# Kernel optimization log

Hardware: AMD Instinct MI355X
Metric: run time of the kernel (lower is better)

Reference implementation:

```python
import jax, jax.numpy as jnp
import numpy as np

H, W = 250, 400
N_RAYS = H * W          # 100000 (one patch)
N_SAMPLES = 1_000_000
P, C, DIM = 50000, 16, 8
STEP_SIZE = 0.005
DENSITY_SHIFT = 0.0
DENSITY_SCALE = min(1.0 / (1.0 - DENSITY_SHIFT), 25.0)


def setup_inputs() -> dict:
    key = jax.random.key(0)
    ks = jax.random.split(key, 12)
    return {
        "trivecs": jax.random.normal(ks[0], (P, C, 3, DIM), dtype=jnp.float32),
        "densities": jax.random.normal(ks[1], (P, C), dtype=jnp.float32),
        "colors": jax.random.normal(ks[2], (P, C, 3), dtype=jnp.float32),
        "local_gweight_s": jax.random.uniform(ks[3], (N_SAMPLES, 3), dtype=jnp.float32),
        "local_gweight_l": jax.random.uniform(ks[4], (N_SAMPLES, 3), dtype=jnp.float32),
        "t_min": jax.random.uniform(ks[5], (N_RAYS,), dtype=jnp.float32),
        "bg": jax.random.uniform(ks[6], (3,), dtype=jnp.float32),
        "local_gindx_s": jax.random.randint(ks[7], (N_SAMPLES, 3), 0, DIM, dtype=jnp.int32),
        "local_gindx_l": jax.random.randint(ks[8], (N_SAMPLES, 3), 0, DIM, dtype=jnp.int32),
        "tensoRF_id": jax.random.randint(ks[9], (N_SAMPLES,), 0, P, dtype=jnp.int32),
        "ray_id": jnp.sort(jax.random.randint(ks[10], (N_SAMPLES,), 0, N_RAYS, dtype=jnp.int32)),
        "step_id": jax.random.randint(ks[11], (N_SAMPLES,), 0, 200, dtype=jnp.int32),
    }


def reference(trivecs, densities, colors, local_gweight_s, local_gweight_l,
              t_min, bg, local_gindx_s, local_gindx_l, tensoRF_id, ray_id, step_id):
    # --- compute_feature: trilinear tensor-decomposition gather ---
    def interp(a):
        vs = trivecs[tensoRF_id, :, a, local_gindx_s[:, a]]  # [N, C]
        vl = trivecs[tensoRF_id, :, a, local_gindx_l[:, a]]  # [N, C]
        return vs * local_gweight_s[:, a:a + 1] + vl * local_gweight_l[:, a:a + 1]

    feature = interp(0) * interp(1) * interp(2)               # [N, C]
    sigma = (feature * densities[tensoRF_id]).sum(axis=1)     # [N]
    color = jnp.einsum('nc,nck->nk', feature, colors[tensoRF_id])  # [N, 3]

    # --- density activation & alpha ---
    density = jax.nn.softplus(sigma - DENSITY_SHIFT * 10.0) * DENSITY_SCALE
    alpha = 1.0 - jnp.exp(-density * STEP_SIZE)               # [N]

    # --- Alphas2Weights: per-ray exclusive transmittance (ray_id sorted) ---
    log_t = -density * STEP_SIZE                              # == log(1 - alpha)
    seg_total = jax.ops.segment_sum(log_t, ray_id, num_segments=N_RAYS)  # [R]
    seg_offset = jnp.concatenate([jnp.zeros((1,), log_t.dtype),
                                  jnp.cumsum(seg_total)[:-1]])           # [R]
    excl = jnp.cumsum(log_t) - log_t - seg_offset[ray_id]     # within-segment excl cumsum
    weights = alpha * jnp.exp(excl)                           # [N]
    bg_weight = jnp.exp(seg_total)                            # [R], prod(1-alpha) per ray

    # --- ray compositing ---
    rgb = jax.nn.sigmoid(color)                               # [N, 3]
    rgb_map = jax.ops.segment_sum(weights[:, None] * rgb, ray_id, num_segments=N_RAYS)
    rgb_map = rgb_map + bg_weight[:, None] * bg[None, :]
    z_val = t_min[ray_id] + step_id.astype(jnp.float32) * STEP_SIZE
    depth_map = jax.ops.segment_sum(weights * z_val, ray_id, num_segments=N_RAYS)
    alpha_map = 1.0 - bg_weight

    rgb_map = rgb_map.T.reshape(3, H, W)
    depth_map = depth_map.reshape(H, W)
    alpha_map = alpha_map.reshape(H, W)
    return rgb_map, depth_map, alpha_map
```

## Files before the change

kernel.cpp:

```cpp
#include <hip/hip_runtime.h>
#include <math.h>

#define HN       250
#define WN       400
#define N_RAYS   (HN * WN)
#define N_SAMP   1000000
#define P_TENSO  50000
#define STEP_SZ  0.005f
#define DENS_SCALE 1.0f
#define NB_SCAN  ((P_TENSO + 1023) / 1024)


#define OFF_PACK    0
#define OFF_RESULTS 32000000
#define OFF_PERM    48000000
#define OFF_RT      52000000
#define OFF_CURSOR  56000000
#define OFF_STARTS  56200000
#define OFF_BSUMS   56400000
#define OFF_FLAG    56400512
#define OFF_RSTART  56401024
#define WS_NEED     (56401024 + 400004 + 64)

#define ROW_STRIDE 20
#define TV_F   (24 * ROW_STRIDE)
#define SLAB_F (TV_F + 16 + 48)

__global__ __launch_bounds__(256) void pack_bounds_rank(
    const int*   __restrict__ tenso_id,
    const int*   __restrict__ ray_id,
    const int*   __restrict__ gis, const int* __restrict__ gil,
    const float* __restrict__ gws, const float* __restrict__ gwl,
    int* __restrict__ cursor,
    int* __restrict__ rt,
    int* __restrict__ ray_start,
    float4* __restrict__ pack)
{
    int n = blockIdx.x * 256 + threadIdx.x;
    if (n >= N_SAMP) return;

    const int tid = tenso_id[n];
    const int rk = atomicAdd(&cursor[tid], 1);
    rt[n] = (tid << 16) | rk;

    unsigned bits = (unsigned)gis[n*3+0] | ((unsigned)gis[n*3+1] << 3) | ((unsigned)gis[n*3+2] << 6)
                  | ((unsigned)gil[n*3+0] << 9) | ((unsigned)gil[n*3+1] << 12) | ((unsigned)gil[n*3+2] << 15);
    float4 A = make_float4(gws[n*3+0], gws[n*3+1], gws[n*3+2], gwl[n*3+0]);
    float4 B = make_float4(gwl[n*3+1], gwl[n*3+2], __uint_as_float(bits), 0.0f);
    pack[(size_t)n * 2 + 0] = A;
    pack[(size_t)n * 2 + 1] = B;

    int r = ray_id[n];
    int rprev = (n == 0) ? -1 : ray_id[n - 1];
    for (int q = rprev + 1; q <= r; ++q) ray_start[q] = n;
    if (n == N_SAMP - 1) {
        for (int q = r + 1; q <= N_RAYS; ++q) ray_start[q] = N_SAMP;
    }
}

__global__ __launch_bounds__(256) void scan_fused(
    const int* __restrict__ cursor,
    int* __restrict__ starts,
    int* __restrict__ bsums,
    int* __restrict__ flag)
{
    __shared__ int lds[257];
    const int b = blockIdx.x;
    const int t = threadIdx.x;
    const int base = b * 1024 + t * 4;

    int v[4]; int s = 0;
    #pragma unroll
    for (int i = 0; i < 4; ++i) {
        int idx = base + i;
        v[i] = (idx < P_TENSO) ? cursor[idx] : 0;
        s += v[i];
    }
    lds[t] = s;
    __syncthreads();
    for (int d = 1; d < 256; d <<= 1) {
        int x = (t >= d) ? lds[t - d] : 0;
        __syncthreads();
        lds[t] += x;
        __syncthreads();
    }
    if (t == 255) bsums[b] = lds[255];

    __threadfence();
    __syncthreads();
    if (t == 0) {
        atomicAdd(flag, 1);
        while (atomicAdd(flag, 0) < gridDim.x) { }
    }
    __syncthreads();
    __threadfence();

    if (t < 64) {
        int x = (t < b) ? bsums[t] : 0;
        #pragma unroll
        for (int m = 1; m < 64; m <<= 1) x += __shfl_xor(x, m);
        if (t == 0) lds[256] = x;
    }
    __syncthreads();
    const int pre = lds[256];

    int run = pre + ((t > 0) ? lds[t - 1] : 0);
    #pragma unroll
    for (int i = 0; i < 4; ++i) {
        int idx = base + i;
        if (idx < P_TENSO) starts[idx] = run;
        run += v[i];
    }
}

__global__ __launch_bounds__(256) void finalize_perm(
    const int* __restrict__ rt,
    const int* __restrict__ starts,
    int* __restrict__ perm)
{
    int n = blockIdx.x * 256 + threadIdx.x;
    if (n >= N_SAMP) return;
    const unsigned w = (unsigned)rt[n];
    int pos = starts[w >> 16] + (int)(w & 0xFFFFu);
    perm[pos] = n;
}

__global__ __launch_bounds__(256) void gather_phase(
    const float* __restrict__ trivecs,
    const float* __restrict__ densities,
    const float* __restrict__ colors,
    const int*   __restrict__ starts,
    const int*   __restrict__ counts,
    const int*   __restrict__ perm,
    const float4* __restrict__ pack,
    float* __restrict__ results_f)
{
    __shared__ __align__(16) float lds[4 * SLAB_F];
    const int lane = threadIdx.x & 63;
    const int wv   = threadIdx.x >> 6;
    const int t    = blockIdx.x * 4 + wv;
    if (t >= P_TENSO) return;

    const int start = starts[t];
    const int cnt   = counts[t];
    if (cnt == 0) return;

    float* slab = lds + wv * SLAB_F;
    float* dl   = slab + TV_F;
    float* cl   = dl + 16;

    const int g = lane >> 2;
    const int j = lane & 3;
    const int end = start + cnt;

    int p = start + g;
    int n = perm[(p < end) ? p : (end - 1)];

    const float* tvg = trivecs + (size_t)t * 384;
    #pragma unroll
    for (int i = 0; i < 6; ++i) {
        int l = lane + i * 64;
        int c = l / 24;
        int rem = l - c * 24;
        slab[rem * ROW_STRIDE + c] = tvg[l];
    }
    if (lane < 16) dl[lane] = densities[(size_t)t * 16 + lane];
    if (lane < 48) {
        int c = lane / 3, k = lane - c * 3;
        cl[k * 16 + c] = colors[(size_t)t * 48 + lane];
    }

    const float4 dens4 = *(const float4*)(dl + 4 * j);
    const float4 col0  = *(const float4*)(cl + 4 * j);
    const float4 col1  = *(const float4*)(cl + 16 + 4 * j);
    const float4 col2  = *(const float4*)(cl + 32 + 4 * j);

    const int niter = (cnt + 15) >> 4;

    for (int it = 0; it < niter; ++it) {
        const bool valid = (p < end);
        const int sn = n;

        const float4 A = pack[(size_t)sn * 2 + 0];
        const float4 B = pack[(size_t)sn * 2 + 1];

        if (it + 1 < niter) {
            p = start + (it + 1) * 16 + g;
            n = perm[(p < end) ? p : (end - 1)];
        }

        const unsigned bits = __float_as_uint(B.z);

        float4 f;
        {
            const int is = bits & 7, il = (bits >> 9) & 7;
            const float4 vs = *(const float4*)(slab + is * ROW_STRIDE + 4 * j);
            const float4 vl = *(const float4*)(slab + il * ROW_STRIDE + 4 * j);
            f.x = vs.x * A.x + vl.x * A.w;
            f.y = vs.y * A.x + vl.y * A.w;
            f.z = vs.z * A.x + vl.z * A.w;
            f.w = vs.w * A.x + vl.w * A.w;
        }
        {
            const int is = (bits >> 3) & 7, il = (bits >> 12) & 7;
            const float4 vs = *(const float4*)(slab + (8 + is) * ROW_STRIDE + 4 * j);
            const float4 vl = *(const float4*)(slab + (8 + il) * ROW_STRIDE + 4 * j);
            f.x *= vs.x * A.y + vl.x * B.x;
            f.y *= vs.y * A.y + vl.y * B.x;
            f.z *= vs.z * A.y + vl.z * B.x;
            f.w *= vs.w * A.y + vl.w * B.x;
        }
        {
            const int is = (bits >> 6) & 7, il = (bits >> 15) & 7;
            const float4 vs = *(const float4*)(slab + (16 + is) * ROW_STRIDE + 4 * j);
            const float4 vl = *(const float4*)(slab + (16 + il) * ROW_STRIDE + 4 * j);
            f.x *= vs.x * A.z + vl.x * B.y;
            f.y *= vs.y * A.z + vl.y * B.y;
            f.z *= vs.z * A.z + vl.z * B.y;
            f.w *= vs.w * A.z + vl.w * B.y;
        }

        float s0 = f.x * dens4.x + f.y * dens4.y + f.z * dens4.z + f.w * dens4.w;
        float s1 = f.x * col0.x  + f.y * col0.y  + f.z * col0.z  + f.w * col0.w;
        float s2 = f.x * col1.x  + f.y * col1.y  + f.z * col1.z  + f.w * col1.w;
        float s3 = f.x * col2.x  + f.y * col2.y  + f.z * col2.z  + f.w * col2.w;

        s0 += __shfl_xor(s0, 1); s0 += __shfl_xor(s0, 2);
        s1 += __shfl_xor(s1, 1); s1 += __shfl_xor(s1, 2);
        s2 += __shfl_xor(s2, 1); s2 += __shfl_xor(s2, 2);
        s3 += __shfl_xor(s3, 1); s3 += __shfl_xor(s3, 2);

        const float sj = (j == 0) ? s0 : (j == 1) ? s1 : (j == 2) ? s2 : s3;
        float val;
        if (j == 0) {
            float dens = fmaxf(sj, 0.0f) + __logf(1.0f + __expf(-fabsf(sj)));
            val = -(dens * DENS_SCALE) * STEP_SZ;
        } else {
            val = 1.0f / (1.0f + __expf(-sj));
        }
        if (valid) results_f[(size_t)sn * 4 + j] = val;
    }
}

__global__ __launch_bounds__(256) void ray_render(
    const float4* __restrict__ results,
    const float*  __restrict__ t_min,
    const float*  __restrict__ bg,
    const int*    __restrict__ ray_start,
    const int*    __restrict__ step_id,
    float* __restrict__ out)
{
    const int lane = threadIdx.x & 63;
    const int g    = lane & 3;
    const int r    = (blockIdx.x * 256 + threadIdx.x) >> 2;
    if (r >= N_RAYS) return;
    const int s = ray_start[r];
    const int e = ray_start[r + 1];
    const float tmin_r = t_min[r];

    float eT = 1.0f, aR = 0.0f, aG = 0.0f, aB = 0.0f, aD = 0.0f;
    const int niter = (e - s + 3) >> 2;
    for (int it = 0; it < niter; ++it) {
        const int idx = s + it * 4 + g;
        const bool valid = (idx < e);
        const int ci = valid ? idx : (e - 1);
        const float4 res = results[ci];
        const float z = tmin_r + (float)step_id[ci] * STEP_SZ;
        const float elt = valid ? __expf(res.x) : 1.0f;

        float excl = 1.0f;
        const float v1 = __shfl_up(elt, 1, 4); if (g >= 1) excl *= v1;
        const float v2 = __shfl_up(elt, 2, 4); if (g >= 2) excl *= v2;
        const float v3 = __shfl_up(elt, 3, 4); if (g >= 3) excl *= v3;

        const float w = eT * excl * (1.0f - elt);
        aR += w * res.y;
        aG += w * res.z;
        aB += w * res.w;
        aD += w * z;

        const float tot = __shfl(excl * elt, 3, 4);
        eT *= tot;
    }

    aR += __shfl_xor(aR, 1); aR += __shfl_xor(aR, 2);
    aG += __shfl_xor(aG, 1); aG += __shfl_xor(aG, 2);
    aB += __shfl_xor(aB, 1); aB += __shfl_xor(aB, 2);
    aD += __shfl_xor(aD, 1); aD += __shfl_xor(aD, 2);

    const float outv = (g == 0) ? aR + eT * bg[0]
                     : (g == 1) ? aG + eT * bg[1]
                     : (g == 2) ? aB + eT * bg[2]
                     : aD;
    out[g * N_RAYS + r] = outv;
    if (g == 0) out[4 * N_RAYS + r] = 1.0f - eT;
}

__global__ __launch_bounds__(256) void trivec_render_fallback(
    const float* __restrict__ trivecs, const float* __restrict__ densities,
    const float* __restrict__ colors, const float* __restrict__ gws,
    const float* __restrict__ gwl, const float* __restrict__ t_min,
    const float* __restrict__ bg, const int* __restrict__ gis,
    const int* __restrict__ gil, const int* __restrict__ tenso_id,
    const int* __restrict__ ray_id, const int* __restrict__ step_id,
    float* __restrict__ out)
{
    const int lane = threadIdx.x & 63;
    const int r = blockIdx.x * 4 + (threadIdx.x >> 6);
    if (r >= N_RAYS) return;
    const int c = lane & 15;
    const int g = lane >> 4;
    int lo = 0, hi = N_SAMP;
    while (lo < hi) { int mid = (lo + hi) >> 1; if (ray_id[mid] < r) lo = mid + 1; else hi = mid; }
    const int seg_start = lo;
    hi = N_SAMP;
    while (lo < hi) { int mid = (lo + hi) >> 1; if (ray_id[mid] < r + 1) lo = mid + 1; else hi = mid; }
    const int seg_end = lo;
    const float tmin_r = t_min[r];
    float Tlog = 0.0f, accR = 0.0f, accG = 0.0f, accB = 0.0f, accD = 0.0f;
    const int niter = (seg_end - seg_start + 3) >> 2;
    for (int it = 0; it < niter; ++it) {
        const int n = seg_start + it * 4 + g;
        const bool valid = (n < seg_end);
        const int nc = valid ? n : (seg_end - 1);
        const int tid = tenso_id[nc];
        const float* tv = trivecs + (size_t)tid * 384 + c * 24;
        float f = 1.0f;
        #pragma unroll
        for (int a = 0; a < 3; ++a) {
            const int is = gis[nc*3+a], il = gil[nc*3+a];
            const float wS = gws[nc*3+a], wL = gwl[nc*3+a];
            f *= (tv[a*8+is] * wS + tv[a*8+il] * wL);
        }
        const float dns = densities[(size_t)tid * 16 + c];
        const float* colp = colors + ((size_t)tid * 16 + c) * 3;
        float s0 = f*dns, s1 = f*colp[0], s2 = f*colp[1], s3 = f*colp[2];
        #pragma unroll
        for (int m = 1; m < 16; m <<= 1) {
            s0 += __shfl_xor(s0, m); s1 += __shfl_xor(s1, m);
            s2 += __shfl_xor(s2, m); s3 += __shfl_xor(s3, m);
        }
        float dens = fmaxf(s0, 0.0f) + __logf(1.0f + __expf(-fabsf(s0)));
        const float lt = valid ? (-dens * STEP_SZ) : 0.0f;
        const float alpha = 1.0f - __expf(lt);
        const float rr = 1.0f/(1.0f+__expf(-s1)), gg = 1.0f/(1.0f+__expf(-s2)), bb = 1.0f/(1.0f+__expf(-s3));
        const float z = tmin_r + (float)step_id[nc] * STEP_SZ;
        const float lt0 = __shfl(lt,0), lt1 = __shfl(lt,16), lt2 = __shfl(lt,32), lt3 = __shfl(lt,48);
        float excl = Tlog;
        if (g > 0) excl += lt0;
        if (g > 1) excl += lt1;
        if (g > 2) excl += lt2;
        const float w = alpha * __expf(excl);
        Tlog += lt0 + lt1 + lt2 + lt3;
        accR += w*rr; accG += w*gg; accB += w*bb; accD += w*z;
    }
    accR += __shfl_xor(accR,16); accR += __shfl_xor(accR,32);
    accG += __shfl_xor(accG,16); accG += __shfl_xor(accG,32);
    accB += __shfl_xor(accB,16); accB += __shfl_xor(accB,32);
    accD += __shfl_xor(accD,16); accD += __shfl_xor(accD,32);
    const float bgw = __expf(Tlog);
    if (lane == 0) {
        out[0*N_RAYS+r] = accR + bgw*bg[0];
        out[1*N_RAYS+r] = accG + bgw*bg[1];
        out[2*N_RAYS+r] = accB + bgw*bg[2];
        out[3*N_RAYS+r] = accD;
        out[4*N_RAYS+r] = 1.0f - bgw;
    }
}

extern "C" void kernel_launch(void* const* d_in, const int* in_sizes, int n_in,
                              void* d_out, int out_size, void* d_ws, size_t ws_size,
                              hipStream_t stream) {
    const float* trivecs   = (const float*)d_in[0];
    const float* densities = (const float*)d_in[1];
    const float* colors    = (const float*)d_in[2];
    const float* gws       = (const float*)d_in[3];
    const float* gwl       = (const float*)d_in[4];
    const float* t_min     = (const float*)d_in[5];
    const float* bg        = (const float*)d_in[6];
    const int*   gis       = (const int*)d_in[7];
    const int*   gil       = (const int*)d_in[8];
    const int*   tenso_id  = (const int*)d_in[9];
    const int*   ray_id    = (const int*)d_in[10];
    const int*   step_id   = (const int*)d_in[11];
    float* out = (float*)d_out;

    if (ws_size < (size_t)WS_NEED) {
        trivec_render_fallback<<<(N_RAYS + 3) / 4, 256, 0, stream>>>(
            trivecs, densities, colors, gws, gwl, t_min, bg,
            gis, gil, tenso_id, ray_id, step_id, out);
        return;
    }

    char* ws = (char*)d_ws;
    float4* pack     = (float4*)(ws + OFF_PACK);
    float4* results  = (float4*)(ws + OFF_RESULTS);
    int*    perm     = (int*)(ws + OFF_PERM);
    int*    rt       = (int*)(ws + OFF_RT);
    int*    cursor   = (int*)(ws + OFF_CURSOR);
    int*    starts   = (int*)(ws + OFF_STARTS);
    int*    bsums    = (int*)(ws + OFF_BSUMS);
    int*    flag     = (int*)(ws + OFF_FLAG);
    int*    raystart = (int*)(ws + OFF_RSTART);

    hipMemsetAsync(ws + OFF_CURSOR, 0, (OFF_FLAG + 64) - OFF_CURSOR, stream);

    pack_bounds_rank<<<(N_SAMP + 255) / 256, 256, 0, stream>>>(
        tenso_id, ray_id, gis, gil, gws, gwl, cursor, rt, raystart, pack);
    scan_fused<<<NB_SCAN, 256, 0, stream>>>(cursor, starts, bsums, flag);
    finalize_perm<<<(N_SAMP + 255) / 256, 256, 0, stream>>>(
        rt, starts, perm);
    gather_phase<<<(P_TENSO + 3) / 4, 256, 0, stream>>>(
        trivecs, densities, colors, starts, cursor, perm, pack, (float*)results);
    ray_render<<<(N_RAYS * 4 + 255) / 256, 256, 0, stream>>>(
        results, t_min, bg, raystart, step_id, out);
}
```

Baseline: 278.5 us.

## Fuse permutation scatter into scan kernel and make gather persistent with prefetch

Folds the permutation scatter into the scan kernel behind a second grid-wide spin barrier, removing one kernel launch. The scan kernel also writes an end sentinel to starts so the gather kernel no longer needs the counts array. The gather kernel becomes persistent: a fixed grid of 2048 blocks loops over tensors, loading the next tensor's vectors, densities, colors and bounds into registers while processing the current one. The ray-boundary pass now gets the previous ray id with a wave shuffle instead of a second global load. The risk is that the fused scatter runs on only about 49 blocks, which sharply cuts parallelism for a 1M-element latency-bound scatter.

```diff
diff --git a/kernel.cpp b/kernel.cpp
--- a/kernel.cpp
+++ b/kernel.cpp
@@ -9,6 +9,8 @@
 #define STEP_SZ  0.005f
 #define DENS_SCALE 1.0f
 #define NB_SCAN  ((P_TENSO + 1023) / 1024)
+#define NB_GATHER 2048
+#define NW_GATHER (NB_GATHER * 4)
 
 
 #define OFF_PACK    0
@@ -17,7 +19,7 @@
 #define OFF_RT      52000000
 #define OFF_CURSOR  56000000
 #define OFF_STARTS  56200000
-#define OFF_BSUMS   56400000
+#define OFF_BSUMS   56400064
 #define OFF_FLAG    56400512
 #define OFF_RSTART  56401024
 #define WS_NEED     (56401024 + 400004 + 64)
@@ -38,6 +40,7 @@
 {
     int n = blockIdx.x * 256 + threadIdx.x;
     if (n >= N_SAMP) return;
+    const int lane = threadIdx.x & 63;
 
     const int tid = tenso_id[n];
     const int rk = atomicAdd(&cursor[tid], 1);
@@ -50,19 +53,24 @@
     pack[(size_t)n * 2 + 0] = A;
     pack[(size_t)n * 2 + 1] = B;
 
-    int r = ray_id[n];
-    int rprev = (n == 0) ? -1 : ray_id[n - 1];
+    const int r = ray_id[n];
+    const int rup = __shfl_up(r, 1);
+    int rprev;
+    if (lane == 0) rprev = (n == 0) ? -1 : ray_id[n - 1];
+    else           rprev = rup;
     for (int q = rprev + 1; q <= r; ++q) ray_start[q] = n;
     if (n == N_SAMP - 1) {
         for (int q = r + 1; q <= N_RAYS; ++q) ray_start[q] = N_SAMP;
     }
 }
 
-__global__ __launch_bounds__(256) void scan_fused(
+__global__ __launch_bounds__(256) void scan_finalize(
     const int* __restrict__ cursor,
+    const int* __restrict__ rt,
     int* __restrict__ starts,
     int* __restrict__ bsums,
-    int* __restrict__ flag)
+    int* __restrict__ flag,
+    int* __restrict__ perm)
 {
     __shared__ int lds[257];
     const int b = blockIdx.x;
@@ -89,8 +97,8 @@
     __threadfence();
     __syncthreads();
     if (t == 0) {
-        atomicAdd(flag, 1);
-        while (atomicAdd(flag, 0) < gridDim.x) { }
+        atomicAdd(&flag[0], 1);
+        while (atomicAdd(&flag[0], 0) < NB_SCAN) { }
     }
     __syncthreads();
     __threadfence();
@@ -110,19 +118,22 @@
         int idx = base + i;
         if (idx < P_TENSO) starts[idx] = run;
         run += v[i];
-    }
-}
-
-__global__ __launch_bounds__(256) void finalize_perm(
-    const int* __restrict__ rt,
-    const int* __restrict__ starts,
-    int* __restrict__ perm)
-{
-    int n = blockIdx.x * 256 + threadIdx.x;
-    if (n >= N_SAMP) return;
-    const unsigned w = (unsigned)rt[n];
-    int pos = starts[w >> 16] + (int)(w & 0xFFFFu);
-    perm[pos] = n;
+        if (idx == P_TENSO - 1) starts[P_TENSO] = run;
+    }
+
+    __threadfence();
+    __syncthreads();
+    if (t == 0) {
+        atomicAdd(&flag[1], 1);
+        while (atomicAdd(&flag[1], 0) < NB_SCAN) { }
+    }
+    __syncthreads();
+    __threadfence();
+
+    for (int n = b * 256 + t; n < N_SAMP; n += NB_SCAN * 256) {
+        const unsigned w = (unsigned)rt[n];
+        perm[starts[w >> 16] + (int)(w & 0xFFFFu)] = n;
+    }
 }
 
 __global__ __launch_bounds__(256) void gather_phase(
@@ -130,7 +141,6 @@
     const float* __restrict__ densities,
     const float* __restrict__ colors,
     const int*   __restrict__ starts,
-    const int*   __restrict__ counts,
     const int*   __restrict__ perm,
     const float4* __restrict__ pack,
     float* __restrict__ results_f)
@@ -138,107 +148,133 @@
     __shared__ __align__(16) float lds[4 * SLAB_F];
     const int lane = threadIdx.x & 63;
     const int wv   = threadIdx.x >> 6;
-    const int t    = blockIdx.x * 4 + wv;
-    if (t >= P_TENSO) return;
-
-    const int start = starts[t];
-    const int cnt   = counts[t];
-    if (cnt == 0) return;
-
     float* slab = lds + wv * SLAB_F;
     float* dl   = slab + TV_F;
     float* cl   = dl + 16;
-
     const int g = lane >> 2;
     const int j = lane & 3;
-    const int end = start + cnt;
-
-    int p = start + g;
-    int n = perm[(p < end) ? p : (end - 1)];
-
-    const float* tvg = trivecs + (size_t)t * 384;
-    #pragma unroll
-    for (int i = 0; i < 6; ++i) {
-        int l = lane + i * 64;
-        int c = l / 24;
-        int rem = l - c * 24;
-        slab[rem * ROW_STRIDE + c] = tvg[l];
-    }
-    if (lane < 16) dl[lane] = densities[(size_t)t * 16 + lane];
-    if (lane < 48) {
-        int c = lane / 3, k = lane - c * 3;
-        cl[k * 16 + c] = colors[(size_t)t * 48 + lane];
-    }
-
-    const float4 dens4 = *(const float4*)(dl + 4 * j);
-    const float4 col0  = *(const float4*)(cl + 4 * j);
-    const float4 col1  = *(const float4*)(cl + 16 + 4 * j);
-    const float4 col2  = *(const float4*)(cl + 32 + 4 * j);
-
-    const int niter = (cnt + 15) >> 4;
-
-    for (int it = 0; it < niter; ++it) {
-        const bool valid = (p < end);
-        const int sn = n;
-
-        const float4 A = pack[(size_t)sn * 2 + 0];
-        const float4 B = pack[(size_t)sn * 2 + 1];
-
-        if (it + 1 < niter) {
-            p = start + (it + 1) * 16 + g;
-            n = perm[(p < end) ? p : (end - 1)];
+
+    int wr0,wr1,wr2,wr3,wr4,wr5;
+    {
+        int l, c, rem;
+        l = lane;       c = l/24; rem = l - c*24; wr0 = rem*ROW_STRIDE + c;
+        l = lane + 64;  c = l/24; rem = l - c*24; wr1 = rem*ROW_STRIDE + c;
+        l = lane + 128; c = l/24; rem = l - c*24; wr2 = rem*ROW_STRIDE + c;
+        l = lane + 192; c = l/24; rem = l - c*24; wr3 = rem*ROW_STRIDE + c;
+        l = lane + 256; c = l/24; rem = l - c*24; wr4 = rem*ROW_STRIDE + c;
+        l = lane + 320; c = l/24; rem = l - c*24; wr5 = rem*ROW_STRIDE + c;
+    }
+    int cli; { int c = lane/3, k = lane - c*3; cli = k*16 + c; }
+
+    int t = blockIdx.x * 4 + wv;
+
+    float v0,v1,v2,v3,v4,v5, vd, vc;
+    {
+        const float* tvg = trivecs + (size_t)t * 384;
+        v0 = tvg[lane];       v1 = tvg[lane + 64];  v2 = tvg[lane + 128];
+        v3 = tvg[lane + 192]; v4 = tvg[lane + 256]; v5 = tvg[lane + 320];
+        vd = (lane < 16) ? densities[(size_t)t * 16 + lane] : 0.0f;
+        vc = (lane < 48) ? colors[(size_t)t * 48 + lane]    : 0.0f;
+    }
+    int st0 = starts[t], st1 = starts[t + 1];
+    slab[wr0]=v0; slab[wr1]=v1; slab[wr2]=v2; slab[wr3]=v3; slab[wr4]=v4; slab[wr5]=v5;
+    if (lane < 16) dl[lane] = vd;
+    if (lane < 48) cl[cli]  = vc;
+
+    for (;;) {
+        const int tn = t + NW_GATHER;
+        const bool hn = (tn < P_TENSO);
+        int stn0 = 0, stn1 = 0;
+        if (hn) {
+            const float* tvn = trivecs + (size_t)tn * 384;
+            v0 = tvn[lane];       v1 = tvn[lane + 64];  v2 = tvn[lane + 128];
+            v3 = tvn[lane + 192]; v4 = tvn[lane + 256]; v5 = tvn[lane + 320];
+            vd = (lane < 16) ? densities[(size_t)tn * 16 + lane] : 0.0f;
+            vc = (lane < 48) ? colors[(size_t)tn * 48 + lane]    : 0.0f;
+            stn0 = starts[tn]; stn1 = starts[tn + 1];
         }
 
-        const unsigned bits = __float_as_uint(B.z);
-
-        float4 f;
-        {
-            const int is = bits & 7, il = (bits >> 9) & 7;
-            const float4 vs = *(const float4*)(slab + is * ROW_STRIDE + 4 * j);
-            const float4 vl = *(const float4*)(slab + il * ROW_STRIDE + 4 * j);
-            f.x = vs.x * A.x + vl.x * A.w;
-            f.y = vs.y * A.x + vl.y * A.w;
-            f.z = vs.z * A.x + vl.z * A.w;
-            f.w = vs.w * A.x + vl.w * A.w;
+        const int start = st0, end = st1, cnt = st1 - st0;
+        if (cnt > 0) {
+            int p = start + g;
+            int n = perm[(p < end) ? p : (end - 1)];
+
+            const float4 dens4 = *(const float4*)(dl + 4 * j);
+            const float4 col0  = *(const float4*)(cl + 4 * j);
+            const float4 col1  = *(const float4*)(cl + 16 + 4 * j);
+            const float4 col2  = *(const float4*)(cl + 32 + 4 * j);
+
+            const int niter = (cnt + 15) >> 4;
+            for (int it = 0; it < niter; ++it) {
+                const bool valid = (p < end);
+                const int sn = n;
+
+                const float4 A = pack[(size_t)sn * 2 + 0];
+                const float4 B = pack[(size_t)sn * 2 + 1];
+
+                if (it + 1 < niter) {
+                    p = start + (it + 1) * 16 + g;
+                    n = perm[(p < end) ? p : (end - 1)];
+                }
+
+                const unsigned bits = __float_as_uint(B.z);
+
+                float4 f;
+                {
+                    const int is = bits & 7, il = (bits >> 9) & 7;
+                    const float4 vs = *(const float4*)(slab + is * ROW_STRIDE + 4 * j);
+                    const float4 vl = *(const float4*)(slab + il * ROW_STRIDE + 4 * j);
+                    f.x = vs.x * A.x + vl.x * A.w;
+                    f.y = vs.y * A.x + vl.y * A.w;
+                    f.z = vs.z * A.x + vl.z * A.w;
+                    f.w = vs.w * A.x + vl.w * A.w;
+                }
+                {
+                    const int is = (bits >> 3) & 7, il = (bits >> 12) & 7;
+                    const float4 vs = *(const float4*)(slab + (8 + is) * ROW_STRIDE + 4 * j);
+                    const float4 vl = *(const float4*)(slab + (8 + il) * ROW_STRIDE + 4 * j);
+                    f.x *= vs.x * A.y + vl.x * B.x;
+                    f.y *= vs.y * A.y + vl.y * B.x;
+                    f.z *= vs.z * A.y + vl.z * B.x;
+                    f.w *= vs.w * A.y + vl.w * B.x;
+                }
+                {
+                    const int is = (bits >> 6) & 7, il = (bits >> 15) & 7;
+                    const float4 vs = *(const float4*)(slab + (16 + is) * ROW_STRIDE + 4 * j);
+                    const float4 vl = *(const float4*)(slab + (16 + il) * ROW_STRIDE + 4 * j);
+                    f.x *= vs.x * A.z + vl.x * B.y;
+                    f.y *= vs.y * A.z + vl.y * B.y;
+                    f.z *= vs.z * A.z + vl.z * B.y;
+                    f.w *= vs.w * A.z + vl.w * B.y;
+                }
+
+                float s0 = f.x * dens4.x + f.y * dens4.y + f.z * dens4.z + f.w * dens4.w;
+                float s1 = f.x * col0.x  + f.y * col0.y  + f.z * col0.z  + f.w * col0.w;
+                float s2 = f.x * col1.x  + f.y * col1.y  + f.z * col1.z  + f.w * col1.w;
+                float s3 = f.x * col2.x  + f.y * col2.y  + f.z * col2.z  + f.w * col2.w;
+
+                s0 += __shfl_xor(s0, 1); s0 += __shfl_xor(s0, 2);
+                s1 += __shfl_xor(s1, 1); s1 += __shfl_xor(s1, 2);
+                s2 += __shfl_xor(s2, 1); s2 += __shfl_xor(s2, 2);
+                s3 += __shfl_xor(s3, 1); s3 += __shfl_xor(s3, 2);
+
+                const float sj = (j == 0) ? s0 : (j == 1) ? s1 : (j == 2) ? s2 : s3;
+                float val;
+                if (j == 0) {
+                    float dens = fmaxf(sj, 0.0f) + __logf(1.0f + __expf(-fabsf(sj)));
+                    val = -(dens * DENS_SCALE) * STEP_SZ;
+                } else {
+                    val = 1.0f / (1.0f + __expf(-sj));
+                }
+                if (valid) results_f[(size_t)sn * 4 + j] = val;
+            }
         }
-        {
-            const int is = (bits >> 3) & 7, il = (bits >> 12) & 7;
-            const float4 vs = *(const float4*)(slab + (8 + is) * ROW_STRIDE + 4 * j);
-            const float4 vl = *(const float4*)(slab + (8 + il) * ROW_STRIDE + 4 * j);
-            f.x *= vs.x * A.y + vl.x * B.x;
-            f.y *= vs.y * A.y + vl.y * B.x;
-            f.z *= vs.z * A.y + vl.z * B.x;
-            f.w *= vs.w * A.y + vl.w * B.x;
-        }
-        {
-            const int is = (bits >> 6) & 7, il = (bits >> 15) & 7;
-            const float4 vs = *(const float4*)(slab + (16 + is) * ROW_STRIDE + 4 * j);
-            const float4 vl = *(const float4*)(slab + (16 + il) * ROW_STRIDE + 4 * j);
-            f.x *= vs.x * A.z + vl.x * B.y;
-            f.y *= vs.y * A.z + vl.y * B.y;
-            f.z *= vs.z * A.z + vl.z * B.y;
-            f.w *= vs.w * A.z + vl.w * B.y;
-        }
-
-        float s0 = f.x * dens4.x + f.y * dens4.y + f.z * dens4.z + f.w * dens4.w;
-        float s1 = f.x * col0.x  + f.y * col0.y  + f.z * col0.z  + f.w * col0.w;
-        float s2 = f.x * col1.x  + f.y * col1.y  + f.z * col1.z  + f.w * col1.w;
-        float s3 = f.x * col2.x  + f.y * col2.y  + f.z * col2.z  + f.w * col2.w;
-
-        s0 += __shfl_xor(s0, 1); s0 += __shfl_xor(s0, 2);
-        s1 += __shfl_xor(s1, 1); s1 += __shfl_xor(s1, 2);
-        s2 += __shfl_xor(s2, 1); s2 += __shfl_xor(s2, 2);
-        s3 += __shfl_xor(s3, 1); s3 += __shfl_xor(s3, 2);
-
-        const float sj = (j == 0) ? s0 : (j == 1) ? s1 : (j == 2) ? s2 : s3;
-        float val;
-        if (j == 0) {
-            float dens = fmaxf(sj, 0.0f) + __logf(1.0f + __expf(-fabsf(sj)));
-            val = -(dens * DENS_SCALE) * STEP_SZ;
-        } else {
-            val = 1.0f / (1.0f + __expf(-sj));
-        }
-        if (valid) results_f[(size_t)sn * 4 + j] = val;
+
+        if (!hn) break;
+        slab[wr0]=v0; slab[wr1]=v1; slab[wr2]=v2; slab[wr3]=v3; slab[wr4]=v4; slab[wr5]=v5;
+        if (lane < 16) dl[lane] = vd;
+        if (lane < 48) cl[cli]  = vc;
+        st0 = stn0; st1 = stn1; t = tn;
     }
 }
 
@@ -407,11 +443,10 @@
 
     pack_bounds_rank<<<(N_SAMP + 255) / 256, 256, 0, stream>>>(
         tenso_id, ray_id, gis, gil, gws, gwl, cursor, rt, raystart, pack);
-    scan_fused<<<NB_SCAN, 256, 0, stream>>>(cursor, starts, bsums, flag);
-    finalize_perm<<<(N_SAMP + 255) / 256, 256, 0, stream>>>(
-        rt, starts, perm);
-    gather_phase<<<(P_TENSO + 3) / 4, 256, 0, stream>>>(
-        trivecs, densities, colors, starts, cursor, perm, pack, (float*)results);
+    scan_finalize<<<NB_SCAN, 256, 0, stream>>>(
+        cursor, rt, starts, bsums, flag, perm);
+    gather_phase<<<NB_GATHER, 256, 0, stream>>>(
+        trivecs, densities, colors, starts, perm, pack, (float*)results);
     ray_render<<<(N_RAYS * 4 + 255) / 256, 256, 0, stream>>>(
         results, t_min, bg, raystart, step_id, out);
 }
```

Measured after the change: 318.5 us. 1.14x slower.

## Process samples with two lanes each instead of four in feature kernel

Applied to the files above, without the earlier changes.

The per-tensoRF feature kernel now assigns 2 lanes per sample, each covering 8 channels, so a wave handles 32 samples per iteration instead of 16. This halves the shuffle reduction steps and iteration count, and writes float2 results instead of scalars. The cost is more registers and LDS reads per lane. The pack kernel also reads the previous ray_id through a wave shuffle instead of a second global load.

```diff
diff --git a/kernel.cpp b/kernel.cpp
--- a/kernel.cpp
+++ b/kernel.cpp
@@ -38,6 +38,7 @@
 {
     int n = blockIdx.x * 256 + threadIdx.x;
     if (n >= N_SAMP) return;
+    const int lane = threadIdx.x & 63;
 
     const int tid = tenso_id[n];
     const int rk = atomicAdd(&cursor[tid], 1);
@@ -50,8 +51,11 @@
     pack[(size_t)n * 2 + 0] = A;
     pack[(size_t)n * 2 + 1] = B;
 
-    int r = ray_id[n];
-    int rprev = (n == 0) ? -1 : ray_id[n - 1];
+    const int r = ray_id[n];
+    const int rup = __shfl_up(r, 1);
+    int rprev;
+    if (lane == 0) rprev = (n == 0) ? -1 : ray_id[n - 1];
+    else           rprev = rup;
     for (int q = rprev + 1; q <= r; ++q) ray_start[q] = n;
     if (n == N_SAMP - 1) {
         for (int q = r + 1; q <= N_RAYS; ++q) ray_start[q] = N_SAMP;
@@ -149,11 +153,12 @@
     float* dl   = slab + TV_F;
     float* cl   = dl + 16;
 
-    const int g = lane >> 2;
-    const int j = lane & 3;
+    const int pr = lane >> 1;
+    const int h  = lane & 1;
+    const int hc = h * 8;
     const int end = start + cnt;
 
-    int p = start + g;
+    int p = start + pr;
     int n = perm[(p < end) ? p : (end - 1)];
 
     const float* tvg = trivecs + (size_t)t * 384;
@@ -170,12 +175,16 @@
         cl[k * 16 + c] = colors[(size_t)t * 48 + lane];
     }
 
-    const float4 dens4 = *(const float4*)(dl + 4 * j);
-    const float4 col0  = *(const float4*)(cl + 4 * j);
-    const float4 col1  = *(const float4*)(cl + 16 + 4 * j);
-    const float4 col2  = *(const float4*)(cl + 32 + 4 * j);
-
-    const int niter = (cnt + 15) >> 4;
+    const float4 dnA = *(const float4*)(dl + hc);
+    const float4 dnB = *(const float4*)(dl + hc + 4);
+    const float4 c0A = *(const float4*)(cl + hc);
+    const float4 c0B = *(const float4*)(cl + hc + 4);
+    const float4 c1A = *(const float4*)(cl + 16 + hc);
+    const float4 c1B = *(const float4*)(cl + 16 + hc + 4);
+    const float4 c2A = *(const float4*)(cl + 32 + hc);
+    const float4 c2B = *(const float4*)(cl + 32 + hc + 4);
+
+    const int niter = (cnt + 31) >> 5;
 
     for (int it = 0; it < niter; ++it) {
         const bool valid = (p < end);
@@ -185,60 +194,83 @@
         const float4 B = pack[(size_t)sn * 2 + 1];
 
         if (it + 1 < niter) {
-            p = start + (it + 1) * 16 + g;
+            p = start + (it + 1) * 32 + pr;
             n = perm[(p < end) ? p : (end - 1)];
         }
 
         const unsigned bits = __float_as_uint(B.z);
 
-        float4 f;
+        float4 fA, fB;
         {
             const int is = bits & 7, il = (bits >> 9) & 7;
-            const float4 vs = *(const float4*)(slab + is * ROW_STRIDE + 4 * j);
-            const float4 vl = *(const float4*)(slab + il * ROW_STRIDE + 4 * j);
-            f.x = vs.x * A.x + vl.x * A.w;
-            f.y = vs.y * A.x + vl.y * A.w;
-            f.z = vs.z * A.x + vl.z * A.w;
-            f.w = vs.w * A.x + vl.w * A.w;
+            const float4 vsA = *(const float4*)(slab + is * ROW_STRIDE + hc);
+            const float4 vsB = *(const float4*)(slab + is * ROW_STRIDE + hc + 4);
+            const float4 vlA = *(const float4*)(slab + il * ROW_STRIDE + hc);
+            const float4 vlB = *(const float4*)(slab + il * ROW_STRIDE + hc + 4);
+            fA.x = vsA.x * A.x + vlA.x * A.w;
+            fA.y = vsA.y * A.x + vlA.y * A.w;
+            fA.z = vsA.z * A.x + vlA.z * A.w;
+            fA.w = vsA.w * A.x + vlA.w * A.w;
+            fB.x = vsB.x * A.x + vlB.x * A.w;
+            fB.y = vsB.y * A.x + vlB.y * A.w;
+            fB.z = vsB.z * A.x + vlB.z * A.w;
+            fB.w = vsB.w * A.x + vlB.w * A.w;
         }
         {
             const int is = (bits >> 3) & 7, il = (bits >> 12) & 7;
-            const float4 vs = *(const float4*)(slab + (8 + is) * ROW_STRIDE + 4 * j);
-            const float4 vl = *(const float4*)(slab + (8 + il) * ROW_STRIDE + 4 * j);
-            f.x *= vs.x * A.y + vl.x * B.x;
-            f.y *= vs.y * A.y + vl.y * B.x;
-            f.z *= vs.z * A.y + vl.z * B.x;
-            f.w *= vs.w * A.y + vl.w * B.x;
+            const float4 vsA = *(const float4*)(slab + (8 + is) * ROW_STRIDE + hc);
+            const float4 vsB = *(const float4*)(slab + (8 + is) * ROW_STRIDE + hc + 4);
+            const float4 vlA = *(const float4*)(slab + (8 + il) * ROW_STRIDE + hc);
+            const float4 vlB = *(const float4*)(slab + (8 + il) * ROW_STRIDE + hc + 4);
+            fA.x *= vsA.x * A.y + vlA.x * B.x;
+            fA.y *= vsA.y * A.y + vlA.y * B.x;
+            fA.z *= vsA.z * A.y + vlA.z * B.x;
+            fA.w *= vsA.w * A.y + vlA.w * B.x;
+            fB.x *= vsB.x * A.y + vlB.x * B.x;
+            fB.y *= vsB.y * A.y + vlB.y * B.x;
+            fB.z *= vsB.z * A.y + vlB.z * B.x;
+            fB.w *= vsB.w * A.y + vlB.w * B.x;
         }
         {
             const int is = (bits >> 6) & 7, il = (bits >> 15) & 7;
-            const float4 vs = *(const float4*)(slab + (16 + is) * ROW_STRIDE + 4 * j);
-            const float4 vl = *(const float4*)(slab + (16 + il) * ROW_STRIDE + 4 * j);
-            f.x *= vs.x * A.z + vl.x * B.y;
-            f.y *= vs.y * A.z + vl.y * B.y;
-            f.z *= vs.z * A.z + vl.z * B.y;
-            f.w *= vs.w * A.z + vl.w * B.y;
-        }
-
-        float s0 = f.x * dens4.x + f.y * dens4.y + f.z * dens4.z + f.w * dens4.w;
-        float s1 = f.x * col0.x  + f.y * col0.y  + f.z * col0.z  + f.w * col0.w;
-        float s2 = f.x * col1.x  + f.y * col1.y  + f.z * col1.z  + f.w * col1.w;
-        float s3 = f.x * col2.x  + f.y * col2.y  + f.z * col2.z  + f.w * col2.w;
-
-        s0 += __shfl_xor(s0, 1); s0 += __shfl_xor(s0, 2);
-        s1 += __shfl_xor(s1, 1); s1 += __shfl_xor(s1, 2);
-        s2 += __shfl_xor(s2, 1); s2 += __shfl_xor(s2, 2);
-        s3 += __shfl_xor(s3, 1); s3 += __shfl_xor(s3, 2);
-
-        const float sj = (j == 0) ? s0 : (j == 1) ? s1 : (j == 2) ? s2 : s3;
-        float val;
-        if (j == 0) {
-            float dens = fmaxf(sj, 0.0f) + __logf(1.0f + __expf(-fabsf(sj)));
-            val = -(dens * DENS_SCALE) * STEP_SZ;
+            const float4 vsA = *(const float4*)(slab + (16 + is) * ROW_STRIDE + hc);
+            const float4 vsB = *(const float4*)(slab + (16 + is) * ROW_STRIDE + hc + 4);
+            const float4 vlA = *(const float4*)(slab + (16 + il) * ROW_STRIDE + hc);
+            const float4 vlB = *(const float4*)(slab + (16 + il) * ROW_STRIDE + hc + 4);
+            fA.x *= vsA.x * A.z + vlA.x * B.y;
+            fA.y *= vsA.y * A.z + vlA.y * B.y;
+            fA.z *= vsA.z * A.z + vlA.z * B.y;
+            fA.w *= vsA.w * A.z + vlA.w * B.y;
+            fB.x *= vsB.x * A.z + vlB.x * B.y;
+            fB.y *= vsB.y * A.z + vlB.y * B.y;
+            fB.z *= vsB.z * A.z + vlB.z * B.y;
+            fB.w *= vsB.w * A.z + vlB.w * B.y;
+        }
+
+        float s0 = fA.x*dnA.x + fA.y*dnA.y + fA.z*dnA.z + fA.w*dnA.w
+                 + fB.x*dnB.x + fB.y*dnB.y + fB.z*dnB.z + fB.w*dnB.w;
+        float s1 = fA.x*c0A.x + fA.y*c0A.y + fA.z*c0A.z + fA.w*c0A.w
+                 + fB.x*c0B.x + fB.y*c0B.y + fB.z*c0B.z + fB.w*c0B.w;
+        float s2 = fA.x*c1A.x + fA.y*c1A.y + fA.z*c1A.z + fA.w*c1A.w
+                 + fB.x*c1B.x + fB.y*c1B.y + fB.z*c1B.z + fB.w*c1B.w;
+        float s3 = fA.x*c2A.x + fA.y*c2A.y + fA.z*c2A.z + fA.w*c2A.w
+                 + fB.x*c2B.x + fB.y*c2B.y + fB.z*c2B.z + fB.w*c2B.w;
+
+        s0 += __shfl_xor(s0, 1);
+        s1 += __shfl_xor(s1, 1);
+        s2 += __shfl_xor(s2, 1);
+        s3 += __shfl_xor(s3, 1);
+
+        float2 val;
+        if (h == 0) {
+            float dens = fmaxf(s0, 0.0f) + __logf(1.0f + __expf(-fabsf(s0)));
+            val.x = -(dens * DENS_SCALE) * STEP_SZ;
+            val.y = 1.0f / (1.0f + __expf(-s1));
         } else {
-            val = 1.0f / (1.0f + __expf(-sj));
-        }
-        if (valid) results_f[(size_t)sn * 4 + j] = val;
+            val.x = 1.0f / (1.0f + __expf(-s2));
+            val.y = 1.0f / (1.0f + __expf(-s3));
+        }
+        if (valid) *(float2*)(results_f + (size_t)sn * 4 + 2 * h) = val;
     }
 }
 
```

Result: no change. 275.2 us (-1.2%).
